# Performance work log

Hardware: AMD Instinct MI355X
Metric: run time of the kernel (lower is better)

The kernel has to match this reference:

```python
import jax, jax.numpy as jnp
import numpy as np

CONFIGS = [(4, 2, 1, 1), (4, 4, 3, 3)]  # (k, stride, pad, dilation) per level


def conv2d(x, w, b, stride=1, pad=1):
    y = jax.lax.conv_general_dilated(x, w, (stride, stride), [(pad, pad), (pad, pad)],
                                     dimension_numbers=('NCHW', 'OIHW', 'NCHW'))
    return y + b[None, :, None, None]


def deform_conv(x, offset, mask, wgt, b, k, stride, pad, dil):
    """Modulated deformable conv v2 (zero padding, bilinear sampling).
    x: [B,Cin,Hin,Win]; offset: [B,2K,H,W] interleaved (dy_i,dx_i); mask: [B,K,H,W]."""
    B, Cin, Hin, Win = x.shape
    _, _, H, W = mask.shape
    K = k * k
    dy = offset[:, 0::2]  # [B,K,H,W]
    dx = offset[:, 1::2]
    ks = jnp.arange(k, dtype=offset.dtype) * dil
    kyf = jnp.repeat(ks, k)  # [K], ky-major to match weight.reshape(Cout,Cin,K)
    kxf = jnp.tile(ks, k)
    oy = jnp.arange(H, dtype=offset.dtype) * stride - pad
    ox = jnp.arange(W, dtype=offset.dtype) * stride - pad
    py = (kyf[:, None] + oy[None, :])[None, :, :, None] + dy  # [B,K,H,W]
    px = (kxf[:, None] + ox[None, :])[None, :, None, :] + dx

    def per_image(img, pyi, pxi, mi):
        imgf = img.reshape(Cin, -1)
        y0 = jnp.floor(pyi)
        x0 = jnp.floor(pxi)
        ly = pyi - y0
        lx = pxi - x0
        y0i = y0.astype(jnp.int32)
        x0i = x0.astype(jnp.int32)

        def corner(yi, xi, wt):
            valid = (yi >= 0) & (yi < Hin) & (xi >= 0) & (xi < Win)
            lin = (jnp.clip(yi, 0, Hin - 1) * Win + jnp.clip(xi, 0, Win - 1)).reshape(-1)
            v = imgf[:, lin].reshape(Cin, K, H, W)
            return v * (wt * valid)[None]

        s = (corner(y0i, x0i, (1 - ly) * (1 - lx))
             + corner(y0i, x0i + 1, (1 - ly) * lx)
             + corner(y0i + 1, x0i, ly * (1 - lx))
             + corner(y0i + 1, x0i + 1, ly * lx))
        return s * mi[None]  # [Cin,K,H,W]

    sampled = jax.vmap(per_image)(x, py, px, mask)  # [B,Cin,K,H,W]
    out = jnp.einsum('bikhw,oik->bohw', sampled, wgt.reshape(wgt.shape[0], Cin, K))
    return out + b[None, :, None, None]


def setup_inputs():
    key = jax.random.key(0)
    ks = jax.random.split(key, 16)
    B, C, H = 4, 256, 40
    K = 16  # k*k with k=4
    dcn_std = 1.0 / np.sqrt(C * K)
    res_std = 1.0 / np.sqrt(C * 9)
    return {
        'f0': jax.random.normal(ks[0], (B, C, H * 4, H * 4), jnp.float32),
        'f1': jax.random.normal(ks[1], (B, C, H * 2, H * 2), jnp.float32),
        'f2': jax.random.normal(ks[2], (B, C, H, H), jnp.float32),
        'com_w0': jax.random.normal(ks[3], (3 * K, C, 3, 3), jnp.float32) * 0.01,
        'com_b0': jax.random.normal(ks[4], (3 * K,), jnp.float32) * 0.01,
        'com_w1': jax.random.normal(ks[5], (3 * K, C, 3, 3), jnp.float32) * 0.01,
        'com_b1': jax.random.normal(ks[6], (3 * K,), jnp.float32) * 0.01,
        'dcn_w0': jax.random.normal(ks[7], (C, C, 4, 4), jnp.float32) * dcn_std,
        'dcn_b0': jnp.zeros((C,), jnp.float32),
        'dcn_w1': jax.random.normal(ks[8], (C, C, 4, 4), jnp.float32) * dcn_std,
        'dcn_b1': jnp.zeros((C,), jnp.float32),
        'res_w': jax.random.normal(ks[9], (C, C, 3, 3), jnp.float32) * res_std,
        'res_b': jnp.zeros((C,), jnp.float32),
    }


def reference(f0, f1, f2, com_w0, com_b0, com_w1, com_b1,
              dcn_w0, dcn_b0, dcn_w1, dcn_b1, res_w, res_b):
    features = [f0, f1, f2]
    com = [(com_w0, com_b0), (com_w1, com_b1)]
    dcn = [(dcn_w0, dcn_b0), (dcn_w1, dcn_b1)]
    repeat, levels = 2, 3
    fh = features[-1]
    f = fh
    for _ in range(repeat):
        for l in range(levels - 1):
            k, s, p, d = CONFIGS[l]
            K = k * k
            om = conv2d(f, com[l][0], com[l][1])
            offset = jnp.concatenate([om[:, :K], om[:, K:2 * K]], axis=1)
            m = jax.nn.sigmoid(om[:, 2 * K:])
            dc = deform_conv(features[levels - 2 - l], offset, m, dcn[l][0], dcn[l][1], k, s, p, d)
            f = jax.nn.relu(dc) + f
    return fh + conv2d(f, res_w, res_b)
```

## Files before the change

### kernel.cpp

```cpp
#include <hip/hip_runtime.h>

#define HW40 1600
typedef unsigned short ushort_t;
typedef __attribute__((ext_vector_type(8))) short short8;
typedef __attribute__((ext_vector_type(4))) short short4v;
typedef __attribute__((ext_vector_type(4))) float f4v;

__device__ __forceinline__ float bu(ushort_t u) {
  union { unsigned i; float f; } x; x.i = ((unsigned)u) << 16; return x.f;
}
__device__ __forceinline__ ushort_t fb(float f) {
  union { float f; unsigned i; } x; x.f = f;
  unsigned r = x.i + 0x7FFFu + ((x.i >> 16) & 1u);
  return (ushort_t)(r >> 16);
}

#define GLD16(g, l)                                                            \
  __builtin_amdgcn_global_load_lds(                                            \
      (const __attribute__((address_space(1))) void*)(g),                      \
      (__attribute__((address_space(3))) void*)(l), 16, 0, 0)

#define PART_STRIDE 1638400

__global__ __launch_bounds__(256) void prep_all(
    const float* __restrict__ com_w0, const float* __restrict__ com_w1,
    const float* __restrict__ res_w, const float* __restrict__ dcn_w0,
    const float* __restrict__ dcn_w1, ushort_t* __restrict__ Acom0,
    ushort_t* __restrict__ Acom1, ushort_t* __restrict__ Ares,
    ushort_t* __restrict__ A0, ushort_t* __restrict__ A1,
    ushort_t* __restrict__ zp) {
  __shared__ float s[4096];
  const int g = blockIdx.x;
  const int t = threadIdx.x;
  if (g < 3456) {
    const float* src; ushort_t* dst; int Cout_src; int base;
    if (g < 576)       { src = com_w0; dst = Acom0; Cout_src = 48;  base = g; }
    else if (g < 1152) { src = com_w1; dst = Acom1; Cout_src = 48;  base = g - 576; }
    else               { src = res_w;  dst = Ares;  Cout_src = 256; base = g - 1152; }
    const int idx = base * 256 + t;
    const int co = idx / 2304;
    const int k  = idx - co * 2304;
    const int cin = k & 255, tap = k >> 8;
    dst[idx] = (co < Cout_src) ? fb(src[(size_t)co * 2304 + cin * 9 + tap]) : (ushort_t)0;
  } else if (g < 3968) {
    const int lg = g - 3456;
    const int co = lg & 255;
    const float* w = (lg < 256) ? dcn_w0 : dcn_w1;
    ushort_t* A = (lg < 256) ? A0 : A1;
    const float4* wp = (const float4*)(w + (size_t)co * 4096);
#pragma unroll
    for (int q = 0; q < 4; ++q) ((float4*)s)[t + q * 256] = wp[t + q * 256];
    __syncthreads();
    const int i = t >> 4, cb = (t & 15) * 16;
    ushort_t tmp[16];
#pragma unroll
    for (int j = 0; j < 16; ++j) tmp[j] = fb(s[(cb + j) * 16 + i]);
    ushort_t* op = A + (size_t)co * 4096 + t * 16;
    ((uint4*)op)[0] = ((uint4*)tmp)[0];
    ((uint4*)op)[1] = ((uint4*)tmp)[1];
  } else {
    zp[t] = 0;
  }
}

template <int SPT>
__device__ __forceinline__ void nhwc_body(const float* __restrict__ x,
                                          ushort_t* __restrict__ xt,
                                          int HW, int s0, int b,
                                          ushort_t (*tile)[264]) {
  const int t = threadIdx.x;
  const int l = t & 63, wv = t >> 6;
  constexpr int LPC = SPT / 4;
  constexpr int CPW = (64 / LPC) * 4;
  constexpr int NIT = 256 / (4 * CPW);
  const int spl = (l & (LPC - 1)) * 4;
  const int cgrp = (l / LPC) * 4;
  const float* xb = x + (size_t)b * 256 * HW + s0 + spl;
#pragma unroll
  for (int it = 0; it < NIT; ++it) {
    const int cb = (it * 4 + wv) * CPW + cgrp;
    const float4 v0 = *(const float4*)(xb + (size_t)(cb + 0) * HW);
    const float4 v1 = *(const float4*)(xb + (size_t)(cb + 1) * HW);
    const float4 v2 = *(const float4*)(xb + (size_t)(cb + 2) * HW);
    const float4 v3 = *(const float4*)(xb + (size_t)(cb + 3) * HW);
    ushort_t p0[4] = {fb(v0.x), fb(v1.x), fb(v2.x), fb(v3.x)};
    ushort_t p1[4] = {fb(v0.y), fb(v1.y), fb(v2.y), fb(v3.y)};
    ushort_t p2[4] = {fb(v0.z), fb(v1.z), fb(v2.z), fb(v3.z)};
    ushort_t p3[4] = {fb(v0.w), fb(v1.w), fb(v2.w), fb(v3.w)};
    *(short4v*)(&tile[spl + 0][cb]) = *(short4v*)p0;
    *(short4v*)(&tile[spl + 1][cb]) = *(short4v*)p1;
    *(short4v*)(&tile[spl + 2][cb]) = *(short4v*)p2;
    *(short4v*)(&tile[spl + 3][cb]) = *(short4v*)p3;
  }
  __syncthreads();
  const int c8 = (t & 31) * 8;
  const int spb = t >> 5;
  ushort_t* ob = xt + ((size_t)b * HW + s0) * 256;
#pragma unroll
  for (int q = 0; q < SPT / 8; ++q) {
    const int sp = spb + q * 8;
    *(short8*)(ob + (size_t)sp * 256 + c8) = *(const short8*)(&tile[sp][c8]);
  }
}

__global__ __launch_bounds__(256) void nhwc_all(const float* __restrict__ f2,
                                                const float* __restrict__ f1,
                                                const float* __restrict__ f0,
                                                ushort_t* __restrict__ ft40,
                                                ushort_t* __restrict__ f1t,
                                                ushort_t* __restrict__ f0t) {
  __shared__ __align__(16) ushort_t tile[128][264];
  const int gx = blockIdx.x;
  if (gx < 800) {
    nhwc_body<128>(f0, f0t, 25600, (gx % 200) * 128, gx / 200, tile);
  } else if (gx < 1000) {
    const int g1 = gx - 800;
    nhwc_body<128>(f1, f1t, 6400, (g1 % 50) * 128, g1 / 50, tile);
  } else {
    const int g2 = gx - 1000;
    nhwc_body<64>(f2, ft40, 1600, (g2 % 25) * 64, g2 / 25, tile);
  }
}

__global__ __launch_bounds__(256) void sample_kernel(
    const ushort_t* __restrict__ xt, const ushort_t* __restrict__ part,
    const float* __restrict__ cbias, ushort_t* __restrict__ colT,
    int Hin, int Win, int stride, int pad, int dil) {
  __shared__ int4  gL[128];
  __shared__ float4 gW[128];
  const int g = blockIdx.x;
  const int work = (g & 7) * 100 + (g >> 3);
  const int b = work / 200;
  const int px0 = (work - b * 200) * 8;
  const int t = threadIdx.x;
  const int HWin = Hin * Win;

  if (t < 128) {
    const int px_l = t & 7, i = t >> 3;
    const int p = px0 + px_l;
    const int n = b * 1600 + p;
    const int ph = p / 40, pw = p - (p / 40) * 40;
    float dy = cbias[2 * i], dx = cbias[2 * i + 1], mzr = cbias[32 + i];
#pragma unroll
    for (int kz = 0; kz < 8; ++kz) {
      const ushort_t* pp = part + (size_t)kz * PART_STRIDE + n;
      dy  += bu(pp[(size_t)(2 * i) * 6400]);
      dx  += bu(pp[(size_t)(2 * i + 1) * 6400]);
      mzr += bu(pp[(size_t)(32 + i) * 6400]);
    }
    float mz = 1.f / (1.f + expf(-mzr));
    float py = (float)(ph * stride - pad + (i >> 2) * dil) + dy;
    float px = (float)(pw * stride - pad + (i & 3) * dil) + dx;
    float y0f = floorf(py), x0f = floorf(px);
    float ly = py - y0f, lx = px - x0f;
    int y0 = (int)y0f, x0 = (int)x0f;
    int y1 = y0 + 1, x1 = x0 + 1;
    float hy = 1.f - ly, hx = 1.f - lx;
    float w00 = hy * hx * mz, w01 = hy * lx * mz;
    float w10 = ly * hx * mz, w11 = ly * lx * mz;
    if (y0 < 0 || y0 >= Hin) { w00 = 0.f; w01 = 0.f; }
    if (y1 < 0 || y1 >= Hin) { w10 = 0.f; w11 = 0.f; }
    if (x0 < 0 || x0 >= Win) { w00 = 0.f; w10 = 0.f; }
    if (x1 < 0 || x1 >= Win) { w01 = 0.f; w11 = 0.f; }
    int cy0 = min(max(y0, 0), Hin - 1), cy1 = min(max(y1, 0), Hin - 1);
    int cx0 = min(max(x0, 0), Win - 1), cx1 = min(max(x1, 0), Win - 1);
    gL[t] = make_int4((cy0 * Win + cx0) * 256, (cy0 * Win + cx1) * 256,
                      (cy1 * Win + cx0) * 256, (cy1 * Win + cx1) * 256);
    gW[t] = make_float4(w00, w01, w10, w11);
  }
  __syncthreads();

  const ushort_t* xtb = xt + (size_t)b * HWin * 256;
  const int wv = t >> 6, l = t & 63;
  const int half = l >> 5;
  const int cin8 = (l & 31) * 8;

#pragma unroll 2
  for (int it = 0; it < 16; ++it) {
    const int pr = it * 8 + wv * 2 + half;
    const int4 G = gL[pr];
    const float4 W = gW[pr];
    short8 c00 = *(const short8*)(xtb + G.x + cin8);
    short8 c01 = *(const short8*)(xtb + G.y + cin8);
    short8 c10 = *(const short8*)(xtb + G.z + cin8);
    short8 c11 = *(const short8*)(xtb + G.w + cin8);
    short8 rr;
#pragma unroll
    for (int j = 0; j < 8; ++j) {
      float v = W.x * bu((ushort_t)c00[j]) + W.y * bu((ushort_t)c01[j]) +
                W.z * bu((ushort_t)c10[j]) + W.w * bu((ushort_t)c11[j]);
      rr[j] = (short)fb(v);
    }
    const int px_l = pr & 7, i = pr >> 3;
    *(short8*)(colT + ((size_t)(b * 1600 + px0 + px_l) * 4096 + i * 256 + cin8)) = rr;
  }
}

__global__ __launch_bounds__(256) void gemm_deform(const ushort_t* __restrict__ A,
                                                   const ushort_t* __restrict__ B,
                                                   ushort_t* __restrict__ part) {
  __shared__ ushort_t sA[128 * 32];
  __shared__ ushort_t sB[128 * 32];
  const int g = blockIdx.x;
  const int id = (g & 7) * 50 + (g >> 3);
  const int mt = id & 1, kz = (id >> 1) & 3, nt = id >> 3;
  const int t = threadIdx.x;
  const int wv = t >> 6, l = t & 63;
  const int wm = wv >> 1, wn = wv & 1;

  f4v acc[4][4];
#pragma unroll
  for (int a = 0; a < 4; ++a)
#pragma unroll
    for (int bb = 0; bb < 4; ++bb) acc[a][bb] = (f4v)(0.f);

  const int ra = t >> 2;
  const int q  = ((t & 3) - (ra >> 1)) & 3;
  const size_t aoff = (size_t)(mt * 128 + ra) * 4096 + q * 8;
  const size_t boff = (size_t)(nt * 128 + ra) * 4096 + q * 8;
  ushort_t* lA = sA + t * 8;
  ushort_t* lB = sB + t * 8;

  int k0 = kz * 1024;
  const int lm = l & 15;
  const int koff = (((l >> 4) + (lm >> 1)) & 3) * 8;

  for (int step = 0; step < 32; ++step, k0 += 32) {
    __syncthreads();
    GLD16(A + aoff + k0, lA);
    GLD16(A + aoff + (size_t)64 * 4096 + k0, lA + 2048);
    GLD16(B + boff + k0, lB);
    GLD16(B + boff + (size_t)64 * 4096 + k0, lB + 2048);
    __syncthreads();
    short8 af[4], bfr[4];
#pragma unroll
    for (int fm = 0; fm < 4; ++fm)
      af[fm] = *(const short8*)(sA + (wm * 64 + fm * 16 + lm) * 32 + koff);
#pragma unroll
    for (int fn = 0; fn < 4; ++fn)
      bfr[fn] = *(const short8*)(sB + (wn * 64 + fn * 16 + lm) * 32 + koff);
#pragma unroll
    for (int fm = 0; fm < 4; ++fm)
#pragma unroll
      for (int fn = 0; fn < 4; ++fn)
        acc[fm][fn] = __builtin_amdgcn_mfma_f32_16x16x32_bf16(af[fm], bfr[fn],
                                                              acc[fm][fn], 0, 0, 0);
  }

  const int row_l = (l >> 4) * 4;
  ushort_t* pb = part + (size_t)kz * PART_STRIDE;
#pragma unroll
  for (int fm = 0; fm < 4; ++fm) {
#pragma unroll
    for (int fn = 0; fn < 4; ++fn) {
      const int n = nt * 128 + wn * 64 + fn * 16 + lm;
#pragma unroll
      for (int r = 0; r < 4; ++r) {
        const int m = mt * 128 + wm * 64 + fm * 16 + row_l + r;
        pb[(size_t)m * 6400 + n] = fb(acc[fm][fn][r]);
      }
    }
  }
}

template <int MTILE, int KZ>
__global__ __launch_bounds__(256) void gemm_conv3(const ushort_t* __restrict__ A,
                                                  const ushort_t* __restrict__ ft,
                                                  const ushort_t* __restrict__ zp,
                                                  ushort_t* __restrict__ part,
                                                  int ksteps) {
  constexpr int FN = (MTILE == 128) ? 4 : 2;
  __shared__ ushort_t sA[MTILE * 32];
  __shared__ ushort_t sB[128 * 32];
  const int g = blockIdx.x;
  const int id = (g & 7) * (gridDim.x >> 3) + (g >> 3);
  const int kz = id % KZ;
  const int r = id / KZ;
  const int mt = (MTILE == 128) ? (r & 1) : 0;
  const int nt = (MTILE == 128) ? (r >> 1) : r;
  const int t = threadIdx.x;
  const int wv = t >> 6, l = t & 63;
  const int wm = (MTILE == 128) ? (wv >> 1) : 0;
  const int wn = (MTILE == 128) ? (wv & 1) : wv;

  f4v acc[4][FN];
#pragma unroll
  for (int a = 0; a < 4; ++a)
#pragma unroll
    for (int bb = 0; bb < FN; ++bb) acc[a][bb] = (f4v)(0.f);

  const int ra = t >> 2;
  const int q  = ((t & 3) - (ra >> 1)) & 3;
  const int qc = q * 8;
  const size_t aoff = (size_t)(mt * MTILE + ra) * 2304 + qc;
  const int n0 = nt * 128 + ra;
  const int n1 = n0 + 64;
  const int b0 = n0 / 1600, p0 = n0 - b0 * 1600;
  const int b1 = n1 / 1600, p1 = n1 - b1 * 1600;
  const int ph0 = p0 / 40, pw0 = p0 - (p0 / 40) * 40;
  const int ph1 = p1 / 40, pw1 = p1 - (p1 / 40) * 40;
  const ushort_t* fp0 = ft + (size_t)n0 * 256 + qc;
  const ushort_t* fp1 = ft + (size_t)n1 * 256 + qc;
  ushort_t* lA = sA + t * 8;
  ushort_t* lB = sB + t * 8;

  int k0 = kz * ksteps * 32;
  const int lm = l & 15;
  const int koff = (((l >> 4) + (lm >> 1)) & 3) * 8;

  for (int step = 0; step < ksteps; ++step, k0 += 32) {
    const int tap = k0 >> 8, c0 = k0 & 255;
    const int ky = tap / 3;
    const int dy = ky - 1, dx = (tap - ky * 3) - 1;
    const int off = (dy * 40 + dx) * 256 + c0;
    const bool ok0 = ((unsigned)(ph0 + dy) < 40u) & ((unsigned)(pw0 + dx) < 40u);
    const bool ok1 = ((unsigned)(ph1 + dy) < 40u) & ((unsigned)(pw1 + dx) < 40u);
    const ushort_t* s0 = ok0 ? (fp0 + off) : zp;
    const ushort_t* s1 = ok1 ? (fp1 + off) : zp;
    __syncthreads();
    GLD16(A + aoff + k0, lA);
    if (MTILE == 128) GLD16(A + aoff + (size_t)64 * 2304 + k0, lA + 2048);
    GLD16(s0, lB);
    GLD16(s1, lB + 2048);
    __syncthreads();
    short8 af[4], bfr[FN];
#pragma unroll
    for (int fm = 0; fm < 4; ++fm)
      af[fm] = *(const short8*)(sA + (wm * 64 + fm * 16 + lm) * 32 + koff);
#pragma unroll
    for (int fn = 0; fn < FN; ++fn)
      bfr[fn] = *(const short8*)(sB + (wn * (16 * FN) + fn * 16 + lm) * 32 + koff);
#pragma unroll
    for (int fm = 0; fm < 4; ++fm)
#pragma unroll
      for (int fn = 0; fn < FN; ++fn)
        acc[fm][fn] = __builtin_amdgcn_mfma_f32_16x16x32_bf16(af[fm], bfr[fn],
                                                              acc[fm][fn], 0, 0, 0);
  }

  const int row_l = (l >> 4) * 4;
  ushort_t* pb = part + (size_t)kz * PART_STRIDE;
#pragma unroll
  for (int fm = 0; fm < 4; ++fm) {
#pragma unroll
    for (int fn = 0; fn < FN; ++fn) {
      const int n = nt * 128 + wn * (16 * FN) + fn * 16 + lm;
#pragma unroll
      for (int r = 0; r < 4; ++r) {
        const int m = mt * MTILE + wm * 64 + fm * 16 + row_l + r;
        pb[(size_t)m * 6400 + n] = fb(acc[fm][fn][r]);
      }
    }
  }
}

template <int NKZ>
__global__ __launch_bounds__(256) void epi_fused(const ushort_t* __restrict__ part,
                                                 const float* __restrict__ bias,
                                                 const float* __restrict__ src,
                                                 float* __restrict__ dst,
                                                 ushort_t* __restrict__ ft, int relu) {
  __shared__ __align__(16) ushort_t tile[32][72];
  const int t = threadIdx.x;
  const int p0 = blockIdx.x * 64, c0 = blockIdx.y * 32, b = blockIdx.z;
  const int co_l = t >> 3, pg = t & 7;
  const int co = c0 + co_l;
  const size_t n = (size_t)b * 1600 + p0 + pg * 8;

  float a[8] = {0.f, 0.f, 0.f, 0.f, 0.f, 0.f, 0.f, 0.f};
#pragma unroll
  for (int kz = 0; kz < NKZ; ++kz) {
    short8 pp = *(const short8*)(part + (size_t)kz * PART_STRIDE + (size_t)co * 6400 + n);
#pragma unroll
    for (int j = 0; j < 8; ++j) a[j] += bu((ushort_t)pp[j]);
  }
  const float bv = bias[co];
  const size_t fo = ((size_t)b * 256 + co) * 1600 + p0 + pg * 8;
  float4 s0 = *(const float4*)(src + fo);
  float4 s1 = *(const float4*)(src + fo + 4);
  const float sv[8] = {s0.x, s0.y, s0.z, s0.w, s1.x, s1.y, s1.z, s1.w};
  float o[8];
#pragma unroll
  for (int j = 0; j < 8; ++j) {
    float v = a[j] + bv;
    if (relu) v = fmaxf(v, 0.f);
    o[j] = v + sv[j];
  }
  float4 o0 = {o[0], o[1], o[2], o[3]};
  float4 o1 = {o[4], o[5], o[6], o[7]};
  *(float4*)(dst + fo) = o0;
  *(float4*)(dst + fo + 4) = o1;

  if (ft) {
    short8 rr;
#pragma unroll
    for (int j = 0; j < 8; ++j) rr[j] = (short)fb(o[j]);
    *(short8*)(&tile[co_l][pg * 8]) = rr;
    __syncthreads();
    const int p_l = t >> 2, cb = (t & 3) * 8;
    short8 v;
#pragma unroll
    for (int j = 0; j < 8; ++j) v[j] = (short)tile[cb + j][p_l];
    *(short8*)(ft + ((size_t)(b * 1600 + p0 + p_l)) * 256 + c0 + cb) = v;
  }
}

extern "C" void kernel_launch(void* const* d_in, const int* in_sizes, int n_in,
                              void* d_out, int out_size, void* d_ws, size_t ws_size,
                              hipStream_t stream) {
  (void)in_sizes; (void)n_in; (void)out_size; (void)ws_size;
  const float* f0     = (const float*)d_in[0];
  const float* f1     = (const float*)d_in[1];
  const float* f2     = (const float*)d_in[2];
  const float* com_w0 = (const float*)d_in[3];
  const float* com_b0 = (const float*)d_in[4];
  const float* com_w1 = (const float*)d_in[5];
  const float* com_b1 = (const float*)d_in[6];
  const float* dcn_w0 = (const float*)d_in[7];
  const float* dcn_b0 = (const float*)d_in[8];
  const float* dcn_w1 = (const float*)d_in[9];
  const float* dcn_b1 = (const float*)d_in[10];
  const float* res_w  = (const float*)d_in[11];
  const float* res_b  = (const float*)d_in[12];
  float* out = (float*)d_out;
  float* ws  = (float*)d_ws;

  float*    fbuf  = ws + 0;
  ushort_t* A0    = (ushort_t*)(ws + 1700000);
  ushort_t* A1    = (ushort_t*)(ws + 2230000);
  ushort_t* Acom0 = (ushort_t*)(ws + 2760000);
  ushort_t* Acom1 = (ushort_t*)(ws + 2840000);
  ushort_t* Ares  = (ushort_t*)(ws + 2920000);
  ushort_t* ft40  = (ushort_t*)(ws + 3220000);
  ushort_t* f1t   = (ushort_t*)(ws + 4050000);
  ushort_t* f0t   = (ushort_t*)(ws + 7330000);
  ushort_t* colT  = (ushort_t*)(ws + 20440000);
  ushort_t* part  = (ushort_t*)(ws + 33550000);
  ushort_t* zp    = (ushort_t*)(ws + 40110000);

  prep_all<<<3969, 256, 0, stream>>>(com_w0, com_w1, res_w, dcn_w0, dcn_w1,
                                     Acom0, Acom1, Ares, A0, A1, zp);
  nhwc_all<<<dim3(1100, 1, 1), 256, 0, stream>>>(f2, f1, f0, ft40, f1t, f0t);

  const float* fsrc = f2;
  for (int s = 0; s < 4; ++s) {
    int l = s & 1;
    gemm_conv3<64, 8><<<400, 256, 0, stream>>>(l ? Acom1 : Acom0, ft40, zp, part, 9);
    if (l == 0) {
      sample_kernel<<<800, 256, 0, stream>>>(f1t, part, com_b0, colT, 80, 80, 2, 1, 1);
    } else {
      sample_kernel<<<800, 256, 0, stream>>>(f0t, part, com_b1, colT, 160, 160, 4, 3, 3);
    }
    gemm_deform<<<400, 256, 0, stream>>>(l ? A1 : A0, colT, part);
    epi_fused<4><<<dim3(25, 8, 4), 256, 0, stream>>>(part, l ? dcn_b1 : dcn_b0, fsrc,
                                                     fbuf, ft40, 1);
    fsrc = fbuf;
  }
  gemm_conv3<128, 8><<<800, 256, 0, stream>>>(Ares, ft40, zp, part, 9);
  epi_fused<8><<<dim3(25, 8, 4), 256, 0, stream>>>(part, res_b, f2, out, nullptr, 0);
}
```

Measured before the change: 517.4 us.

## Double-buffer LDS tiles in deform and conv3 GEMMs to overlap loads with MFMA

```diff
diff --git a/kernel.cpp b/kernel.cpp
--- a/kernel.cpp
+++ b/kernel.cpp
@@ -199,8 +199,8 @@
 __global__ __launch_bounds__(256) void gemm_deform(const ushort_t* __restrict__ A,
                                                    const ushort_t* __restrict__ B,
                                                    ushort_t* __restrict__ part) {
-  __shared__ ushort_t sA[128 * 32];
-  __shared__ ushort_t sB[128 * 32];
+  __shared__ ushort_t sA[2][128 * 32];
+  __shared__ ushort_t sB[2][128 * 32];
   const int g = blockIdx.x;
   const int id = (g & 7) * 50 + (g >> 3);
   const int mt = id & 1, kz = (id >> 1) & 3, nt = id >> 3;
@@ -218,27 +218,34 @@
   const int q  = ((t & 3) - (ra >> 1)) & 3;
   const size_t aoff = (size_t)(mt * 128 + ra) * 4096 + q * 8;
   const size_t boff = (size_t)(nt * 128 + ra) * 4096 + q * 8;
-  ushort_t* lA = sA + t * 8;
-  ushort_t* lB = sB + t * 8;
-
-  int k0 = kz * 1024;
+
+  const int k0 = kz * 1024;
   const int lm = l & 15;
   const int koff = (((l >> 4) + (lm >> 1)) & 3) * 8;
 
-  for (int step = 0; step < 32; ++step, k0 += 32) {
+  GLD16(A + aoff + k0, &sA[0][t * 8]);
+  GLD16(A + aoff + (size_t)64 * 4096 + k0, &sA[0][t * 8 + 2048]);
+  GLD16(B + boff + k0, &sB[0][t * 8]);
+  GLD16(B + boff + (size_t)64 * 4096 + k0, &sB[0][t * 8 + 2048]);
+
+  for (int step = 0; step < 32; ++step) {
     __syncthreads();
-    GLD16(A + aoff + k0, lA);
-    GLD16(A + aoff + (size_t)64 * 4096 + k0, lA + 2048);
-    GLD16(B + boff + k0, lB);
-    GLD16(B + boff + (size_t)64 * 4096 + k0, lB + 2048);
-    __syncthreads();
+    const int cur = step & 1;
+    if (step < 31) {
+      const int kn = k0 + (step + 1) * 32;
+      const int nb = cur ^ 1;
+      GLD16(A + aoff + kn, &sA[nb][t * 8]);
+      GLD16(A + aoff + (size_t)64 * 4096 + kn, &sA[nb][t * 8 + 2048]);
+      GLD16(B + boff + kn, &sB[nb][t * 8]);
+      GLD16(B + boff + (size_t)64 * 4096 + kn, &sB[nb][t * 8 + 2048]);
+    }
     short8 af[4], bfr[4];
 #pragma unroll
     for (int fm = 0; fm < 4; ++fm)
-      af[fm] = *(const short8*)(sA + (wm * 64 + fm * 16 + lm) * 32 + koff);
+      af[fm] = *(const short8*)(&sA[cur][(wm * 64 + fm * 16 + lm) * 32 + koff]);
 #pragma unroll
     for (int fn = 0; fn < 4; ++fn)
-      bfr[fn] = *(const short8*)(sB + (wn * 64 + fn * 16 + lm) * 32 + koff);
+      bfr[fn] = *(const short8*)(&sB[cur][(wn * 64 + fn * 16 + lm) * 32 + koff]);
 #pragma unroll
     for (int fm = 0; fm < 4; ++fm)
 #pragma unroll
@@ -270,8 +277,9 @@
                                                   ushort_t* __restrict__ part,
                                                   int ksteps) {
   constexpr int FN = (MTILE == 128) ? 4 : 2;
-  __shared__ ushort_t sA[MTILE * 32];
-  __shared__ ushort_t sB[128 * 32];
+  constexpr int ASZ = MTILE * 32;
+  __shared__ ushort_t sA[2][ASZ];
+  __shared__ ushort_t sB[2][128 * 32];
   const int g = blockIdx.x;
   const int id = (g & 7) * (gridDim.x >> 3) + (g >> 3);
   const int kz = id % KZ;
@@ -301,15 +309,13 @@
   const int ph1 = p1 / 40, pw1 = p1 - (p1 / 40) * 40;
   const ushort_t* fp0 = ft + (size_t)n0 * 256 + qc;
   const ushort_t* fp1 = ft + (size_t)n1 * 256 + qc;
-  ushort_t* lA = sA + t * 8;
-  ushort_t* lB = sB + t * 8;
-
-  int k0 = kz * ksteps * 32;
+
   const int lm = l & 15;
   const int koff = (((l >> 4) + (lm >> 1)) & 3) * 8;
-
-  for (int step = 0; step < ksteps; ++step, k0 += 32) {
-    const int tap = k0 >> 8, c0 = k0 & 255;
+  const int kbase = kz * ksteps * 32;
+
+  auto stage = [&](int kk, int buf) {
+    const int tap = kk >> 8, c0 = kk & 255;
     const int ky = tap / 3;
     const int dy = ky - 1, dx = (tap - ky * 3) - 1;
     const int off = (dy * 40 + dx) * 256 + c0;
@@ -317,19 +323,24 @@
     const bool ok1 = ((unsigned)(ph1 + dy) < 40u) & ((unsigned)(pw1 + dx) < 40u);
     const ushort_t* s0 = ok0 ? (fp0 + off) : zp;
     const ushort_t* s1 = ok1 ? (fp1 + off) : zp;
+    GLD16(A + aoff + kk, &sA[buf][t * 8]);
+    if (MTILE == 128) GLD16(A + aoff + (size_t)64 * 2304 + kk, &sA[buf][t * 8 + 2048]);
+    GLD16(s0, &sB[buf][t * 8]);
+    GLD16(s1, &sB[buf][t * 8 + 2048]);
+  };
+
+  stage(kbase, 0);
+  for (int step = 0; step < ksteps; ++step) {
     __syncthreads();
-    GLD16(A + aoff + k0, lA);
-    if (MTILE == 128) GLD16(A + aoff + (size_t)64 * 2304 + k0, lA + 2048);
-    GLD16(s0, lB);
-    GLD16(s1, lB + 2048);
-    __syncthreads();
+    const int cur = step & 1;
+    if (step < ksteps - 1) stage(kbase + (step + 1) * 32, cur ^ 1);
     short8 af[4], bfr[FN];
 #pragma unroll
     for (int fm = 0; fm < 4; ++fm)
-      af[fm] = *(const short8*)(sA + (wm * 64 + fm * 16 + lm) * 32 + koff);
+      af[fm] = *(const short8*)(&sA[cur][(wm * 64 + fm * 16 + lm) * 32 + koff]);
 #pragma unroll
     for (int fn = 0; fn < FN; ++fn)
-      bfr[fn] = *(const short8*)(sB + (wn * (16 * FN) + fn * 16 + lm) * 32 + koff);
+      bfr[fn] = *(const short8*)(&sB[cur][(wn * (16 * FN) + fn * 16 + lm) * 32 + koff]);
 #pragma unroll
     for (int fm = 0; fm < 4; ++fm)
 #pragma unroll
```

Measured after the change: 534.4 us. +3.3%, slower.
